# Kernel optimization log

Measured on AMD Instinct MI355X. Metric: run time of the kernel, lower is better.

Reference implementation:

```python
import jax, jax.numpy as jnp
import numpy as np

N_QUBITS = 12
K_STEPS = 6
VOCAB = 32000
D_EMB = 512
N_CLASSES = 8
B = 256
SEQ = 128
DIM = 2 ** N_QUBITS


def apply_1q(psi, U, q):
    # psi: [B, 2^n]; U: [2,2] (shared) or [B,2,2] (per-sample). Apply on wire q
    # (PennyLane convention: wire 0 = most significant axis).
    b = psi.shape[0]
    left, right = 2 ** q, 2 ** (N_QUBITS - q - 1)
    st = psi.reshape(b, left, 2, right)
    if U.ndim == 3:
        st = jnp.einsum('bij,bajr->bair', U, st)
    else:
        st = jnp.einsum('ij,bajr->bair', U, st)
    return st.reshape(b, DIM)


def apply_cnot(psi, c, t):
    b = psi.shape[0]
    st = psi.reshape((b,) + (2,) * N_QUBITS)
    c_ax, t_ax = 1 + c, 1 + t
    c0 = jnp.take(st, 0, axis=c_ax)
    c1 = jnp.take(st, 1, axis=c_ax)
    t_ax2 = t_ax - 1 if t_ax > c_ax else t_ax  # axis shift after take
    c1 = jnp.flip(c1, axis=t_ax2)
    return jnp.stack([c0, c1], axis=c_ax).reshape(b, DIM)


def ry_mat(angle):
    # angle: [B] -> [B,2,2] complex64
    c = jnp.cos(angle / 2)
    s = jnp.sin(angle / 2)
    row0 = jnp.stack([c, -s], axis=-1)
    row1 = jnp.stack([s, c], axis=-1)
    return jnp.stack([row0, row1], axis=-2).astype(jnp.complex64)


def rot_mat(phi, theta, omega):
    # PennyLane Rot(phi, theta, omega) = RZ(omega) RY(theta) RZ(phi)
    c = jnp.cos(theta / 2)
    s = jnp.sin(theta / 2)
    ep = jnp.exp(-0.5j * (phi + omega).astype(jnp.complex64))
    em = jnp.exp(0.5j * (phi - omega).astype(jnp.complex64))
    m = jnp.stack([jnp.stack([ep * c, -em * s]), jnp.stack([jnp.conj(em) * s, jnp.conj(ep) * c])])
    return m.astype(jnp.complex64)


def block(psi, x, theta_k):
    # data reupload RY(x_i), trainable Rot, ring of CNOTs (noiseless)
    for i in range(N_QUBITS):
        psi = apply_1q(psi, ry_mat(x[:, i]), i)
    for i in range(N_QUBITS):
        psi = apply_1q(psi, rot_mat(theta_k[i, 0], theta_k[i, 1], theta_k[i, 2]), i)
    for i in range(N_QUBITS - 1):
        psi = apply_cnot(psi, i, i + 1)
    psi = apply_cnot(psi, N_QUBITS - 1, 0)
    return psi


def z_expvals(psi):
    # <Z_i> for all wires from |psi|^2
    b = psi.shape[0]
    p = (psi.real ** 2 + psi.imag ** 2).reshape((b,) + (2,) * N_QUBITS)
    zs = []
    for i in range(N_QUBITS):
        axes = tuple(ax for ax in range(1, N_QUBITS + 1) if ax != 1 + i)
        m = p.sum(axis=axes)  # [B,2]
        zs.append(m[:, 0] - m[:, 1])
    return jnp.stack(zs, axis=-1)  # [B, n_qubits]


def _forward(input_ids, attention_mask, emb_table, proj_w, proj_b, theta, head_w, head_b):
    # encoder: embed -> masked mean pool -> tanh(linear) * pi
    e = emb_table[input_ids]                              # [B,S,D]
    mask = attention_mask[:, :, None].astype(jnp.float32)
    pooled = (e * mask).sum(axis=1) / jnp.clip(mask.sum(axis=1), 1.0)
    x = jnp.tanh(pooled @ proj_w.T + proj_b) * jnp.float32(np.pi)  # [B, n_qubits]

    b = x.shape[0]
    psi = jnp.zeros((b, DIM), jnp.complex64).at[:, 0].set(1.0)
    readouts = []
    for k in range(K_STEPS):
        psi = block(psi, x, theta[k])
        readouts.append(z_expvals(psi))
    step_readouts = jnp.stack(readouts, axis=0)           # [K,B,n_qubits]
    step_logits = step_readouts @ head_w.T + head_b       # [K,B,n_classes]
    return step_logits, step_readouts, step_logits[-1]


def setup_inputs() -> dict:
    key = jax.random.key(0)
    ks = jax.random.split(key, 6)
    input_ids = jax.random.randint(ks[0], (B, SEQ), 0, VOCAB)
    attention_mask = jnp.ones((B, SEQ), dtype=jnp.int32)
    emb_table = jax.random.normal(ks[1], (VOCAB, D_EMB), jnp.float32)
    emb_table = emb_table.at[0].set(0.0)  # padding_idx=0 row is zeros
    proj_w = jax.random.normal(ks[2], (N_QUBITS, D_EMB), jnp.float32) / np.sqrt(D_EMB)
    proj_b = jnp.zeros((N_QUBITS,), jnp.float32)
    theta = 0.01 * jax.random.normal(ks[3], (K_STEPS, N_QUBITS, 3), jnp.float32)
    head_w = jax.random.normal(ks[4], (N_CLASSES, N_QUBITS), jnp.float32) / np.sqrt(N_QUBITS)
    head_b = jnp.zeros((N_CLASSES,), jnp.float32)
    return {'input_ids': input_ids, 'attention_mask': attention_mask,
            'emb_table': emb_table, 'proj_w': proj_w, 'proj_b': proj_b,
            'theta': theta, 'head_w': head_w, 'head_b': head_b}


def reference(input_ids, attention_mask, emb_table, proj_w, proj_b, theta, head_w, head_b):
    return _forward(input_ids, attention_mask, emb_table, proj_w, proj_b, theta, head_w, head_b)
```

## Files before the change

kernel.cpp:

```cpp
#include <hip/hip_runtime.h>
#include <math.h>

#define NQ 12
#define DIM 4096
#define KS 6
#define BB 256
#define SEQ 128
#define DEMB 512


#define REG_GATE(P, W) { \
    float4 c0 = *(const float4*)&s_u[k][W][0]; \
    float4 c1 = *(const float4*)&s_u[k][W][4]; \
    float u00r=c0.x,u00i=c0.y,u01r=c0.z,u01i=c0.w; \
    float u10r=c1.x,u10i=c1.y,u11r=c1.z,u11i=c1.w; \
    _Pragma("unroll") \
    for (int r0 = 0; r0 < 8; ++r0) if (!(r0 & (1 << (P)))) { \
        int r1 = r0 | (1 << (P)); \
        float2 A = a[r0], Bv = a[r1]; \
        a[r0].x = u00r*A.x - u00i*A.y + u01r*Bv.x - u01i*Bv.y; \
        a[r0].y = u00r*A.y + u00i*A.x + u01r*Bv.y + u01i*Bv.x; \
        a[r1].x = u10r*A.x - u10i*A.y + u11r*Bv.x - u11i*Bv.y; \
        a[r1].y = u10r*A.y + u10i*A.x + u11r*Bv.y + u11i*Bv.x; \
    } }

#define BF_PLAIN(v, m) { float p_ = __shfl_xor(v, m, 64); v = v + p_; }
#define BF_SIGN(v, m)  { float p_ = __shfl_xor(v, m, 64); float d_ = v - p_; \
                         v = (lane & m) ? -d_ : d_; }

#define WAVE_FENCE() asm volatile("s_waitcnt lgkmcnt(0)" ::: "memory")

__device__ __forceinline__ int swz14(int x) { return x ^ ((x >> 4) & 14); }

__global__ __launch_bounds__(512) void fused_kernel(
    const int* __restrict__ ids, const int* __restrict__ mask,
    const float* __restrict__ emb, const float* __restrict__ pw,
    const float* __restrict__ pb, const float* __restrict__ theta,
    const float* __restrict__ hw, const float* __restrict__ hb,
    float* __restrict__ readouts, float* __restrict__ logits,
    float* __restrict__ last)
{
    __shared__ __align__(16) float2 buf0[DIM];
    __shared__ __align__(16) float2 buf1[DIM];
    __shared__ __align__(16) float  s_u[KS][NQ][8];
    __shared__ float  s_red[8][NQ];
    __shared__ float  s_msum[4];
    __shared__ float  s_wred[2][NQ];
    __shared__ float  s_x[NQ];
    __shared__ float  s_hw[8 * NQ];
    __shared__ float  s_hb[8];

    int b = blockIdx.x;
    int tid = threadIdx.x;
    int lane = tid & 63, wave = tid >> 6;

    int*   s_ids = (int*)buf1;
    float* s_m   = (float*)buf1 + SEQ;
    float4* s_part = (float4*)buf0;

    if (tid < SEQ) {
        s_ids[tid] = ids[b * SEQ + tid];
        s_m[tid]   = (float)mask[b * SEQ + tid];
    }
    if (tid >= 256 && tid < 256 + 8 * NQ) s_hw[tid - 256] = hw[tid - 256];
    if (tid >= 384 && tid < 392)          s_hb[tid - 384] = hb[tid - 384];
    __syncthreads();

    {
        int g = tid >> 7, e = tid & 127;
        float4 acc = make_float4(0.f, 0.f, 0.f, 0.f);
        float msum = 0.f;
        #pragma unroll 4
        for (int s = g; s < SEQ; s += 4) {
            float m = s_m[s];
            float4 v = ((const float4*)emb)[(size_t)s_ids[s] * 128 + e];
            acc.x = fmaf(m, v.x, acc.x);
            acc.y = fmaf(m, v.y, acc.y);
            acc.z = fmaf(m, v.z, acc.z);
            acc.w = fmaf(m, v.w, acc.w);
            msum += m;
        }
        __syncthreads();
        s_part[g * 128 + e] = acc;
        if (e == 0) s_msum[g] = msum;
    }
    __syncthreads();

    if (tid < 128) {
        float tm = fmaxf(s_msum[0] + s_msum[1] + s_msum[2] + s_msum[3], 1.f);
        float inv = 1.f / tm;
        float4 p0 = s_part[0 * 128 + tid], p1 = s_part[1 * 128 + tid];
        float4 p2 = s_part[2 * 128 + tid], p3 = s_part[3 * 128 + tid];
        float4 p;
        p.x = (p0.x + p1.x + p2.x + p3.x) * inv;
        p.y = (p0.y + p1.y + p2.y + p3.y) * inv;
        p.z = (p0.z + p1.z + p2.z + p3.z) * inv;
        p.w = (p0.w + p1.w + p2.w + p3.w) * inv;
        float z[NQ];
        #pragma unroll
        for (int i = 0; i < NQ; ++i) {
            float4 w4 = ((const float4*)pw)[i * 128 + tid];
            z[i] = p.x * w4.x + p.y * w4.y + p.z * w4.z + p.w * w4.w;
        }
        #pragma unroll
        for (int i = 0; i < NQ; ++i) {
            #pragma unroll
            for (int off = 32; off > 0; off >>= 1)
                z[i] += __shfl_xor(z[i], off, 64);
        }
        if ((tid & 63) == 0) {
            int w = tid >> 6;
            #pragma unroll
            for (int i = 0; i < NQ; ++i) s_wred[w][i] = z[i];
        }
    }
    __syncthreads();
    if (tid < NQ) {
        float d = pb[tid] + s_wred[0][tid] + s_wred[1][tid];
        s_x[tid] = tanhf(d) * 3.14159274101257324f;
    }
    __syncthreads();

    if (tid < KS * NQ) {
        int k = tid / NQ, w = tid % NQ;
        float ang = s_x[w];
        float cy = cosf(0.5f * ang), sy = sinf(0.5f * ang);
        const float* th = theta + (k * NQ + w) * 3;
        float phi = th[0], te = th[1], om = th[2];
        float ct = cosf(0.5f * te), st = sinf(0.5f * te);
        float a1 = -0.5f * (phi + om);
        float epr = cosf(a1), epi = sinf(a1);
        float a2 = 0.5f * (phi - om);
        float emr = cosf(a2), emi = sinf(a2);
        float R00r = epr * ct,  R00i = epi * ct;
        float R01r = -emr * st, R01i = -emi * st;
        float R10r = emr * st,  R10i = -emi * st;
        float R11r = epr * ct,  R11i = -epi * ct;
        s_u[k][w][0] =  R00r * cy + R01r * sy;
        s_u[k][w][1] =  R00i * cy + R01i * sy;
        s_u[k][w][2] = -R00r * sy + R01r * cy;
        s_u[k][w][3] = -R00i * sy + R01i * cy;
        s_u[k][w][4] =  R10r * cy + R11r * sy;
        s_u[k][w][5] =  R10i * cy + R11i * sy;
        s_u[k][w][6] = -R10r * sy + R11r * cy;
        s_u[k][w][7] = -R10i * sy + R11i * cy;
    }

    int T8 = tid << 3;
    int baseA  = swz14(T8);
    int baseA4 = baseA >> 1;
    int addrB[8], addrC[8], addrD[8], idxP[8];
    #pragma unroll
    for (int r = 0; r < 8; ++r) {
        addrB[r] = swz14((lane & 7) + 8 * r + 64 * (lane >> 3) + 512 * wave);
        addrC[r] = swz14(lane + 64 * r + 512 * wave);
        int jD   = lane + 64 * wave + 512 * r;
        addrD[r] = swz14(jD);
        int b0 = (jD >> 11) & 1;
        int pref = b0, outv = 0;
        for (int w = 1; w < NQ; ++w) {
            pref ^= (jD >> (11 - w)) & 1;
            outv |= pref << (11 - w);
        }
        outv |= (b0 ^ pref) << 11;
        idxP[r] = swz14(outv);
    }
    int w0b = wave & 1, w1b = (wave >> 1) & 1, w2b = (wave >> 2) & 1;
    int wall = w0b ^ w1b ^ w2b;

    float2 a[8];
    #pragma unroll
    for (int r = 0; r < 8; ++r) a[r] = make_float2(0.f, 0.f);
    if (tid == 0) a[0].x = 1.f;
    __syncthreads();

    for (int k = 0; k < KS; ++k) {
        REG_GATE(0, 11) REG_GATE(1, 10) REG_GATE(2, 9)

        #pragma unroll
        for (int i = 0; i < 4; ++i)
            ((float4*)buf0)[baseA4 ^ i] =
                make_float4(a[2*i].x, a[2*i].y, a[2*i+1].x, a[2*i+1].y);
        WAVE_FENCE();
        #pragma unroll
        for (int r = 0; r < 8; ++r) a[r] = buf0[addrB[r]];

        REG_GATE(0, 8) REG_GATE(1, 7) REG_GATE(2, 6)

        #pragma unroll
        for (int r = 0; r < 8; ++r) buf0[addrB[r]] = a[r];
        WAVE_FENCE();
        #pragma unroll
        for (int r = 0; r < 8; ++r) a[r] = buf0[addrC[r]];

        REG_GATE(0, 5) REG_GATE(1, 4) REG_GATE(2, 3)

        #pragma unroll
        for (int r = 0; r < 8; ++r) buf0[addrC[r]] = a[r];
        __syncthreads();
        #pragma unroll
        for (int r = 0; r < 8; ++r) a[r] = buf0[addrD[r]];

        REG_GATE(0, 2) REG_GATE(1, 1) REG_GATE(2, 0)

        #pragma unroll
        for (int r = 0; r < 8; ++r) buf1[idxP[r]] = a[r];

        {
            float p[8];
            #pragma unroll
            for (int r = 0; r < 8; ++r)
                p[r] = a[r].x * a[r].x + a[r].y * a[r].y;
            float Q1 = (p[0]+p[1]+p[6]+p[7]) - (p[2]+p[3]+p[4]+p[5]);
            float Q2 = (p[0]+p[3]+p[5]+p[6]) - (p[1]+p[2]+p[4]+p[7]);
            float Q0 = (p[0]+p[3]+p[4]+p[7]) - (p[1]+p[2]+p[5]+p[6]);
            float q1 = Q1, q2p = Q2, q0 = Q0;
            BF_PLAIN(q1,32) BF_PLAIN(q1,16) BF_PLAIN(q1,8)
            BF_PLAIN(q1,4)  BF_PLAIN(q1,2)  BF_PLAIN(q1,1)
            BF_PLAIN(q2p,32) BF_PLAIN(q2p,16) BF_PLAIN(q2p,8)
            BF_PLAIN(q2p,4)  BF_PLAIN(q2p,2)  BF_PLAIN(q2p,1)
            BF_SIGN(q0,32) BF_SIGN(q0,16) BF_SIGN(q0,8)
            BF_SIGN(q0,4)  BF_SIGN(q0,2)  BF_SIGN(q0,1)
            float c = Q2;
            BF_SIGN(c,32);
            float w6v = c; BF_PLAIN(w6v,16) BF_PLAIN(w6v,8) BF_PLAIN(w6v,4)
                           BF_PLAIN(w6v,2)  BF_PLAIN(w6v,1)
            BF_SIGN(c,16);
            float w7v = c; BF_PLAIN(w7v,8) BF_PLAIN(w7v,4)
                           BF_PLAIN(w7v,2) BF_PLAIN(w7v,1)
            BF_SIGN(c,8);
            float w8v = c; BF_PLAIN(w8v,4) BF_PLAIN(w8v,2) BF_PLAIN(w8v,1)
            BF_SIGN(c,4);
            float w9v = c; BF_PLAIN(w9v,2) BF_PLAIN(w9v,1)
            BF_SIGN(c,2);
            float w10v = c; BF_PLAIN(w10v,1)
            BF_SIGN(c,1);
            if (lane == 0) {
                float* sr = s_red[wave];
                sr[0]  = wall ? -q0  : q0;
                sr[1]  = q1;
                sr[2]  = q2p;
                sr[3]  = w2b ? -q2p : q2p;
                sr[4]  = (w1b ^ w2b) ? -q2p : q2p;
                sr[5]  = wall ? -q2p : q2p;
                sr[6]  = wall ? -w6v : w6v;
                sr[7]  = wall ? -w7v : w7v;
                sr[8]  = wall ? -w8v : w8v;
                sr[9]  = wall ? -w9v : w9v;
                sr[10] = wall ? -w10v : w10v;
                sr[11] = wall ? -c   : c;
            }
        }

        __syncthreads();
        #pragma unroll
        for (int i = 0; i < 4; ++i) {
            float4 v = ((float4*)buf1)[baseA4 ^ i];
            a[2*i]   = make_float2(v.x, v.y);
            a[2*i+1] = make_float2(v.z, v.w);
        }

        if (tid < NQ) {
            float s = 0.f;
            #pragma unroll
            for (int w2 = 0; w2 < 8; ++w2) s += s_red[w2][tid];
            readouts[(k * BB + b) * NQ + tid] = s;
        }
        if (tid < 8) {
            float acc2 = s_hb[tid];
            #pragma unroll
            for (int i = 0; i < NQ; ++i) {
                float si = 0.f;
                #pragma unroll
                for (int w2 = 0; w2 < 8; ++w2) si += s_red[w2][i];
                acc2 = fmaf(si, s_hw[tid * NQ + i], acc2);
            }
            logits[(k * BB + b) * 8 + tid] = acc2;
            if (k == KS - 1) last[b * 8 + tid] = acc2;
        }
    }
}

extern "C" void kernel_launch(void* const* d_in, const int* in_sizes, int n_in,
                              void* d_out, int out_size, void* d_ws, size_t ws_size,
                              hipStream_t stream) {
    const int*   ids   = (const int*)d_in[0];
    const int*   mask  = (const int*)d_in[1];
    const float* emb   = (const float*)d_in[2];
    const float* pw    = (const float*)d_in[3];
    const float* pb    = (const float*)d_in[4];
    const float* theta = (const float*)d_in[5];
    const float* hw    = (const float*)d_in[6];
    const float* hb    = (const float*)d_in[7];
    float* out = (float*)d_out;

    float* readouts = out + KS * BB * 8;
    float* last     = out + KS * BB * 8 + KS * BB * NQ;

    fused_kernel<<<BB, 512, 0, stream>>>(ids, mask, emb, pw, pb, theta,
                                         hw, hb, readouts, out, last);
}
```

Before: 139.9 us.

## Replace LDS transposes with cross-lane shuffle gates and defer readout reduction

Gates on qubits whose index bits live in lane bits now exchange amplitudes with DPP/shuffle xor instead of round-tripping through shared memory. This cuts the four LDS transposes per step to two, using a new wave/lane/register mapping. The Z-expectation reduction moves to the start of the next step, with its global writes after the barrier, so it overlaps with gate work; the last step is handled after the loop. The cost is many more cross-lane shuffles and select logic, and the embedding loop unroll rises from 4 to 8.

```diff
diff --git a/kernel.cpp b/kernel.cpp
--- a/kernel.cpp
+++ b/kernel.cpp
@@ -24,11 +24,24 @@
         a[r1].y = u10r*A.y + u10i*A.x + u11r*Bv.y + u11i*Bv.x; \
     } }
 
-#define BF_PLAIN(v, m) { float p_ = __shfl_xor(v, m, 64); v = v + p_; }
-#define BF_SIGN(v, m)  { float p_ = __shfl_xor(v, m, 64); float d_ = v - p_; \
-                         v = (lane & m) ? -d_ : d_; }
-
-#define WAVE_FENCE() asm volatile("s_waitcnt lgkmcnt(0)" ::: "memory")
+#define SHUF_GATE(MK, W) { \
+    float4 c0 = *(const float4*)&s_u[k][W][0]; \
+    float4 c1 = *(const float4*)&s_u[k][W][4]; \
+    int bit_ = (lane & (MK)) != 0; \
+    float c0r = bit_ ? c1.z : c0.x; \
+    float c0i = bit_ ? c1.w : c0.y; \
+    float c1r = bit_ ? c1.x : c0.z; \
+    float c1i = bit_ ? c1.y : c0.w; \
+    _Pragma("unroll") \
+    for (int r = 0; r < 8; ++r) { \
+        float px = __shfl_xor(a[r].x, MK, 64); \
+        float py = __shfl_xor(a[r].y, MK, 64); \
+        float nx = c0r*a[r].x - c0i*a[r].y + c1r*px - c1i*py; \
+        float ny = c0r*a[r].y + c0i*a[r].x + c1r*py + c1i*px; \
+        a[r].x = nx; a[r].y = ny; \
+    } }
+
+#define PL(v, m) v += __shfl_xor(v, m, 64);
 
 __device__ __forceinline__ int swz14(int x) { return x ^ ((x >> 4) & 14); }
 
@@ -70,7 +83,7 @@
         int g = tid >> 7, e = tid & 127;
         float4 acc = make_float4(0.f, 0.f, 0.f, 0.f);
         float msum = 0.f;
-        #pragma unroll 4
+        #pragma unroll 8
         for (int s = g; s < SEQ; s += 4) {
             float m = s_m[s];
             float4 v = ((const float4*)emb)[(size_t)s_ids[s] * 128 + e];
@@ -149,24 +162,20 @@
     int T8 = tid << 3;
     int baseA  = swz14(T8);
     int baseA4 = baseA >> 1;
-    int addrB[8], addrC[8], addrD[8], idxP[8];
+    int addrE[8], idxP[8];
     #pragma unroll
     for (int r = 0; r < 8; ++r) {
-        addrB[r] = swz14((lane & 7) + 8 * r + 64 * (lane >> 3) + 512 * wave);
-        addrC[r] = swz14(lane + 64 * r + 512 * wave);
-        int jD   = lane + 64 * wave + 512 * r;
-        addrD[r] = swz14(jD);
-        int b0 = (jD >> 11) & 1;
+        int jE = wave | (lane << 3) | (r << 9);
+        addrE[r] = swz14(jE);
+        int b0 = (jE >> 11) & 1;
         int pref = b0, outv = 0;
         for (int w = 1; w < NQ; ++w) {
-            pref ^= (jD >> (11 - w)) & 1;
+            pref ^= (jE >> (11 - w)) & 1;
             outv |= pref << (11 - w);
         }
         outv |= (b0 ^ pref) << 11;
         idxP[r] = swz14(outv);
     }
-    int w0b = wave & 1, w1b = (wave >> 1) & 1, w2b = (wave >> 2) & 1;
-    int wall = w0b ^ w1b ^ w2b;
 
     float2 a[8];
     #pragma unroll
@@ -175,83 +184,80 @@
     __syncthreads();
 
     for (int k = 0; k < KS; ++k) {
-        REG_GATE(0, 11) REG_GATE(1, 10) REG_GATE(2, 9)
-
-        #pragma unroll
-        for (int i = 0; i < 4; ++i)
-            ((float4*)buf0)[baseA4 ^ i] =
-                make_float4(a[2*i].x, a[2*i].y, a[2*i+1].x, a[2*i+1].y);
-        WAVE_FENCE();
-        #pragma unroll
-        for (int r = 0; r < 8; ++r) a[r] = buf0[addrB[r]];
-
-        REG_GATE(0, 8) REG_GATE(1, 7) REG_GATE(2, 6)
-
-        #pragma unroll
-        for (int r = 0; r < 8; ++r) buf0[addrB[r]] = a[r];
-        WAVE_FENCE();
-        #pragma unroll
-        for (int r = 0; r < 8; ++r) a[r] = buf0[addrC[r]];
-
-        REG_GATE(0, 5) REG_GATE(1, 4) REG_GATE(2, 3)
-
-        #pragma unroll
-        for (int r = 0; r < 8; ++r) buf0[addrC[r]] = a[r];
-        __syncthreads();
-        #pragma unroll
-        for (int r = 0; r < 8; ++r) a[r] = buf0[addrD[r]];
-
-        REG_GATE(0, 2) REG_GATE(1, 1) REG_GATE(2, 0)
-
-        #pragma unroll
-        for (int r = 0; r < 8; ++r) buf1[idxP[r]] = a[r];
-
-        {
+        if (k > 0) {
             float p[8];
             #pragma unroll
             for (int r = 0; r < 8; ++r)
                 p[r] = a[r].x * a[r].x + a[r].y * a[r].y;
-            float Q1 = (p[0]+p[1]+p[6]+p[7]) - (p[2]+p[3]+p[4]+p[5]);
-            float Q2 = (p[0]+p[3]+p[5]+p[6]) - (p[1]+p[2]+p[4]+p[7]);
-            float Q0 = (p[0]+p[3]+p[4]+p[7]) - (p[1]+p[2]+p[5]+p[6]);
-            float q1 = Q1, q2p = Q2, q0 = Q0;
-            BF_PLAIN(q1,32) BF_PLAIN(q1,16) BF_PLAIN(q1,8)
-            BF_PLAIN(q1,4)  BF_PLAIN(q1,2)  BF_PLAIN(q1,1)
-            BF_PLAIN(q2p,32) BF_PLAIN(q2p,16) BF_PLAIN(q2p,8)
-            BF_PLAIN(q2p,4)  BF_PLAIN(q2p,2)  BF_PLAIN(q2p,1)
-            BF_SIGN(q0,32) BF_SIGN(q0,16) BF_SIGN(q0,8)
-            BF_SIGN(q0,4)  BF_SIGN(q0,2)  BF_SIGN(q0,1)
-            float c = Q2;
-            BF_SIGN(c,32);
-            float w6v = c; BF_PLAIN(w6v,16) BF_PLAIN(w6v,8) BF_PLAIN(w6v,4)
-                           BF_PLAIN(w6v,2)  BF_PLAIN(w6v,1)
-            BF_SIGN(c,16);
-            float w7v = c; BF_PLAIN(w7v,8) BF_PLAIN(w7v,4)
-                           BF_PLAIN(w7v,2) BF_PLAIN(w7v,1)
-            BF_SIGN(c,8);
-            float w8v = c; BF_PLAIN(w8v,4) BF_PLAIN(w8v,2) BF_PLAIN(w8v,1)
-            BF_SIGN(c,4);
-            float w9v = c; BF_PLAIN(w9v,2) BF_PLAIN(w9v,1)
-            BF_SIGN(c,2);
-            float w10v = c; BF_PLAIN(w10v,1)
-            BF_SIGN(c,1);
+            float e0=p[0]+p[1], d0=p[0]-p[1], e1=p[2]+p[3], d1=p[2]-p[3];
+            float e2=p[4]+p[5], d2=p[4]-p[5], e3=p[6]+p[7], d3=p[6]-p[7];
+            float T   = e0+e1+e2+e3;
+            float S11 = d0+d1+d2+d3;
+            float S10 = (e0-e1)+(e2-e3);
+            float S9  = (e0+e1)-(e2+e3);
+            float c = T, x;
+            x = __shfl_xor(c,1,64);  float V8=(lane&1)? x-c:c-x;  c+=x;
+            PL(V8,2) PL(V8,4) PL(V8,8) PL(V8,16) PL(V8,32)
+            x = __shfl_xor(c,2,64);  float V7=(lane&2)? x-c:c-x;  c+=x;
+            PL(V7,4) PL(V7,8) PL(V7,16) PL(V7,32)
+            x = __shfl_xor(c,4,64);  float V6=(lane&4)? x-c:c-x;  c+=x;
+            PL(V6,8) PL(V6,16) PL(V6,32)
+            x = __shfl_xor(c,8,64);  float V5=(lane&8)? x-c:c-x;  c+=x;
+            PL(V5,16) PL(V5,32)
+            x = __shfl_xor(c,16,64); float V4=(lane&16)? x-c:c-x; c+=x;
+            PL(V4,32)
+            x = __shfl_xor(c,32,64); float V3=(lane&32)? x-c:c-x; c+=x;
+            PL(S11,1) PL(S11,2) PL(S11,4) PL(S11,8) PL(S11,16) PL(S11,32)
+            PL(S10,1) PL(S10,2) PL(S10,4) PL(S10,8) PL(S10,16) PL(S10,32)
+            PL(S9,1)  PL(S9,2)  PL(S9,4)  PL(S9,8)  PL(S9,16)  PL(S9,32)
             if (lane == 0) {
                 float* sr = s_red[wave];
-                sr[0]  = wall ? -q0  : q0;
-                sr[1]  = q1;
-                sr[2]  = q2p;
-                sr[3]  = w2b ? -q2p : q2p;
-                sr[4]  = (w1b ^ w2b) ? -q2p : q2p;
-                sr[5]  = wall ? -q2p : q2p;
-                sr[6]  = wall ? -w6v : w6v;
-                sr[7]  = wall ? -w7v : w7v;
-                sr[8]  = wall ? -w8v : w8v;
-                sr[9]  = wall ? -w9v : w9v;
-                sr[10] = wall ? -w10v : w10v;
-                sr[11] = wall ? -c   : c;
+                sr[11] = S11; sr[10] = S10; sr[9] = S9;
+                sr[8] = V8; sr[7] = V7; sr[6] = V6;
+                sr[5] = V5; sr[4] = V4; sr[3] = V3;
+                sr[2] = (wave & 1) ? -c : c;
+                sr[1] = (wave & 2) ? -c : c;
+                sr[0] = (wave & 4) ? -c : c;
             }
         }
 
+        REG_GATE(0, 11) REG_GATE(1, 10) REG_GATE(2, 9)
+        SHUF_GATE(1, 8) SHUF_GATE(2, 7) SHUF_GATE(4, 6)
+
+        #pragma unroll
+        for (int i = 0; i < 4; ++i)
+            ((float4*)buf0)[baseA4 ^ i] =
+                make_float4(a[2*i].x, a[2*i].y, a[2*i+1].x, a[2*i+1].y);
+        __syncthreads();
+
+        if (k > 0) {
+            if (tid < NQ) {
+                float s = 0.f;
+                #pragma unroll
+                for (int w2 = 0; w2 < 8; ++w2) s += s_red[w2][tid];
+                readouts[((k-1) * BB + b) * NQ + tid] = s;
+            }
+            if (tid < 8) {
+                float acc2 = s_hb[tid];
+                #pragma unroll
+                for (int i = 0; i < NQ; ++i) {
+                    float si = 0.f;
+                    #pragma unroll
+                    for (int w2 = 0; w2 < 8; ++w2) si += s_red[w2][i];
+                    acc2 = fmaf(si, s_hw[tid * NQ + i], acc2);
+                }
+                logits[((k-1) * BB + b) * 8 + tid] = acc2;
+            }
+        }
+
+        #pragma unroll
+        for (int r = 0; r < 8; ++r) a[r] = buf0[addrE[r]];
+
+        REG_GATE(0, 2) REG_GATE(1, 1) REG_GATE(2, 0)
+        SHUF_GATE(8, 5) SHUF_GATE(16, 4) SHUF_GATE(32, 3)
+
+        #pragma unroll
+        for (int r = 0; r < 8; ++r) buf1[idxP[r]] = a[r];
         __syncthreads();
         #pragma unroll
         for (int i = 0; i < 4; ++i) {
@@ -259,25 +265,62 @@
             a[2*i]   = make_float2(v.x, v.y);
             a[2*i+1] = make_float2(v.z, v.w);
         }
-
-        if (tid < NQ) {
-            float s = 0.f;
+    }
+
+    {
+        float p[8];
+        #pragma unroll
+        for (int r = 0; r < 8; ++r)
+            p[r] = a[r].x * a[r].x + a[r].y * a[r].y;
+        float e0=p[0]+p[1], d0=p[0]-p[1], e1=p[2]+p[3], d1=p[2]-p[3];
+        float e2=p[4]+p[5], d2=p[4]-p[5], e3=p[6]+p[7], d3=p[6]-p[7];
+        float T   = e0+e1+e2+e3;
+        float S11 = d0+d1+d2+d3;
+        float S10 = (e0-e1)+(e2-e3);
+        float S9  = (e0+e1)-(e2+e3);
+        float c = T, x;
+        x = __shfl_xor(c,1,64);  float V8=(lane&1)? x-c:c-x;  c+=x;
+        PL(V8,2) PL(V8,4) PL(V8,8) PL(V8,16) PL(V8,32)
+        x = __shfl_xor(c,2,64);  float V7=(lane&2)? x-c:c-x;  c+=x;
+        PL(V7,4) PL(V7,8) PL(V7,16) PL(V7,32)
+        x = __shfl_xor(c,4,64);  float V6=(lane&4)? x-c:c-x;  c+=x;
+        PL(V6,8) PL(V6,16) PL(V6,32)
+        x = __shfl_xor(c,8,64);  float V5=(lane&8)? x-c:c-x;  c+=x;
+        PL(V5,16) PL(V5,32)
+        x = __shfl_xor(c,16,64); float V4=(lane&16)? x-c:c-x; c+=x;
+        PL(V4,32)
+        x = __shfl_xor(c,32,64); float V3=(lane&32)? x-c:c-x; c+=x;
+        PL(S11,1) PL(S11,2) PL(S11,4) PL(S11,8) PL(S11,16) PL(S11,32)
+        PL(S10,1) PL(S10,2) PL(S10,4) PL(S10,8) PL(S10,16) PL(S10,32)
+        PL(S9,1)  PL(S9,2)  PL(S9,4)  PL(S9,8)  PL(S9,16)  PL(S9,32)
+        if (lane == 0) {
+            float* sr = s_red[wave];
+            sr[11] = S11; sr[10] = S10; sr[9] = S9;
+            sr[8] = V8; sr[7] = V7; sr[6] = V6;
+            sr[5] = V5; sr[4] = V4; sr[3] = V3;
+            sr[2] = (wave & 1) ? -c : c;
+            sr[1] = (wave & 2) ? -c : c;
+            sr[0] = (wave & 4) ? -c : c;
+        }
+    }
+    __syncthreads();
+    if (tid < NQ) {
+        float s = 0.f;
+        #pragma unroll
+        for (int w2 = 0; w2 < 8; ++w2) s += s_red[w2][tid];
+        readouts[((KS-1) * BB + b) * NQ + tid] = s;
+    }
+    if (tid < 8) {
+        float acc2 = s_hb[tid];
+        #pragma unroll
+        for (int i = 0; i < NQ; ++i) {
+            float si = 0.f;
             #pragma unroll
-            for (int w2 = 0; w2 < 8; ++w2) s += s_red[w2][tid];
-            readouts[(k * BB + b) * NQ + tid] = s;
-        }
-        if (tid < 8) {
-            float acc2 = s_hb[tid];
-            #pragma unroll
-            for (int i = 0; i < NQ; ++i) {
-                float si = 0.f;
-                #pragma unroll
-                for (int w2 = 0; w2 < 8; ++w2) si += s_red[w2][i];
-                acc2 = fmaf(si, s_hw[tid * NQ + i], acc2);
-            }
-            logits[(k * BB + b) * 8 + tid] = acc2;
-            if (k == KS - 1) last[b * 8 + tid] = acc2;
-        }
+            for (int w2 = 0; w2 < 8; ++w2) si += s_red[w2][i];
+            acc2 = fmaf(si, s_hw[tid * NQ + i], acc2);
+        }
+        logits[((KS-1) * BB + b) * 8 + tid] = acc2;
+        last[b * 8 + tid] = acc2;
     }
 }
 
```

Result: slower. 144.7 us (+3.5%).
